# Kernel tuning notes

Measured on AMD Instinct MI355X. Metric: run time of the kernel, lower is better.

## Reference

```python
import jax, jax.numpy as jnp
import numpy as np

NB, T, NS, NC = 512, 128, 32, 16
NSC = NS + NC


def setup_inputs() -> dict:
    key = jax.random.key(0)
    k1, k2, k3, k4, k5, k6 = jax.random.split(key, 6)
    # Q must be PSD per-step (as in the pypose example: Q = Q.mT @ Q), plus a
    # small ridge so Quu is well-conditioned for pinv.
    Qr = jax.random.normal(k1, (NB, T, NSC, NSC), jnp.float32)
    Q = jnp.einsum('btji,btjk->btik', Qr, Qr) / NSC + 0.1 * jnp.eye(NSC, dtype=jnp.float32)
    p = jax.random.normal(k2, (NB, T, NSC), jnp.float32)
    # Mildly stable LTI dynamics so the T=128 rollout stays bounded.
    A0 = 0.5 * jnp.eye(NS, dtype=jnp.float32) + 0.1 * jax.random.normal(k3, (NS, NS), jnp.float32) / np.sqrt(NS)
    A = jnp.broadcast_to(A0, (NB, NS, NS)).astype(jnp.float32)
    Bm = jax.random.normal(k4, (NB, NS, NC), jnp.float32) / np.sqrt(NS)
    c1 = jax.random.normal(k5, (NB, NS), jnp.float32)
    x_init = jax.random.normal(k6, (NB, NS), jnp.float32)
    return {"x_init": x_init, "Q": Q, "p": p, "A": A, "Bm": Bm, "c1": c1}


def _bmv(M, v):
    return jnp.einsum('bij,bj->bi', M, v)


def reference(x_init, Q, p, A, Bm, c1):
    # F = [A B] : [NB, NS, NSC] (time-invariant LTI system)
    F = jnp.concatenate([A, Bm], axis=-1)
    FT = jnp.swapaxes(F, -1, -2)

    Qtm = jnp.moveaxis(Q, 1, 0)  # [T, NB, NSC, NSC]
    ptm = jnp.moveaxis(p, 1, 0)  # [T, NB, NSC]

    # ---- backward Riccati recursion (t = T-1 .. 0) ----
    def bwd_step(carry, inp):
        V, v = carry  # V: [NB,NS,NS], v: [NB,NS]; zero at t = T-1
        Qt_in, pt = inp
        Qt = Qt_in + FT @ V @ F
        qt = pt + _bmv(FT, v) + _bmv(FT, _bmv(V, c1))
        Qxx, Qxu = Qt[..., :NS, :NS], Qt[..., :NS, NS:]
        Qux, Quu = Qt[..., NS:, :NS], Qt[..., NS:, NS:]
        qx, qu = qt[..., :NS], qt[..., NS:]
        Quu_inv = jnp.linalg.pinv(Quu)
        Kt = -(Quu_inv @ Qux)                 # [NB, NC, NS]
        kt = -_bmv(Quu_inv, qu)               # [NB, NC]
        KtT = jnp.swapaxes(Kt, -1, -2)
        V_new = Qxx + Qxu @ Kt + KtT @ Qux + KtT @ Quu @ Kt
        v_new = qx + _bmv(Qxu, kt) + _bmv(KtT, qu) + _bmv(KtT @ Quu, kt)
        return (V_new, v_new), (Kt, kt)

    V0 = jnp.zeros((NB, NS, NS), Q.dtype)
    v0 = jnp.zeros((NB, NS), Q.dtype)
    _, (Ks, ks) = jax.lax.scan(bwd_step, (V0, v0), (Qtm, ptm), reverse=True)

    # ---- forward rollout (t = 0 .. T-1) ----
    def fwd_step(x, inp):
        Kt, kt, Qt, pt = inp
        ut = _bmv(Kt, x) + kt
        xu = jnp.concatenate([x, ut], axis=-1)
        x_next = _bmv(A, x) + _bmv(Bm, ut) + c1
        c = 0.5 * jnp.einsum('bi,bij,bj->b', xu, Qt, xu) + jnp.sum(xu * pt, axis=-1)
        return x_next, (x, ut, c)

    _, (xs, us, cs) = jax.lax.scan(fwd_step, x_init, (Ks, ks, Qtm, ptm))
    x = jnp.moveaxis(xs, 0, 1)   # [NB, T, NS], states x_0..x_{T-1}
    u = jnp.moveaxis(us, 0, 1)   # [NB, T, NC]
    cost = jnp.sum(cs, axis=0)   # [NB]
    return x, u, cost
```

## Files before the change

kernel.cpp:

```cpp
#include <hip/hip_runtime.h>

#define NB 512
#define T 128
#define NS 32
#define NC 16
#define NSC 48
#define PF 52
#define PV 36
#define PK 36

__device__ __forceinline__ float4 ld4(const float* p) { return *(const float4*)p; }
__device__ __forceinline__ void st4(float* p, float4 v) { *(float4*)p = v; }
__device__ __forceinline__ void fma4(float4& a, float s, float4 f) {
    a.x = fmaf(s, f.x, a.x); a.y = fmaf(s, f.y, a.y);
    a.z = fmaf(s, f.z, a.z); a.w = fmaf(s, f.w, a.w);
}
__device__ __forceinline__ float dot4(float4 a, float4 b) {
    return fmaf(a.x, b.x, fmaf(a.y, b.y, fmaf(a.z, b.z, a.w * b.w)));
}

__global__ __launch_bounds__(256, 2)
void lqr_backward(const float* __restrict__ Q,
                  const float* __restrict__ p,
                  const float* __restrict__ A,
                  const float* __restrict__ Bm,
                  const float* __restrict__ c1,
                  float* __restrict__ Kws,
                  float* __restrict__ kws)
{
    const int b = blockIdx.x;
    const int tid = threadIdx.x;
    const int lane = tid & 63;
    const int wv = tid >> 6;

    __shared__ __align__(16) float sF[NS][PF];
    __shared__ __align__(16) float sW[NS][PF];
    __shared__ __align__(16) float sQt[NSC][PF];
    __shared__ __align__(16) float sV[NS][PV];
    __shared__ __align__(16) float sKt[NC][PK];
    __shared__ __align__(16) float sz[NS];
    __shared__ __align__(16) float sqt[NSC];
    __shared__ __align__(16) float sv[NS];
    __shared__ __align__(16) float sc1[NS];
    __shared__ __align__(16) float skt[NC];

    for (int e = tid; e < NS * NSC; e += 256) {
        int i = e / NSC, j = e % NSC;
        sF[i][j] = (j < NS) ? A[(size_t)b * NS * NS + i * NS + j]
                            : Bm[(size_t)b * NS * NC + i * NC + (j - NS)];
    }
    for (int e = tid; e < NS * NS; e += 256) sV[e >> 5][e & 31] = 0.f;
    if (tid < NS) { sv[tid] = 0.f; sc1[tid] = c1[(size_t)b * NS + tid]; }
    __syncthreads();

    for (int t = T - 1; t >= 0; --t) {
        const float* Qg = Q + ((size_t)b * T + t) * NSC * NSC;

        float4 qgb0 = {0,0,0,0}, qgb1 = {0,0,0,0};
        float preg = 0.f;
        if (tid < 96) {
            int i0b = NS + (tid / 12) * 2, j0b = (tid % 12) * 4;
            qgb0 = ld4(Qg + i0b * NSC + j0b);
            qgb1 = ld4(Qg + (i0b + 1) * NSC + j0b);
        }
        if (tid >= 96 && tid < 144) preg = p[((size_t)b * T + t) * NSC + (tid - 96)];
        if (tid < 192) {
            const int i0 = (tid / 12) * 2, j0 = (tid % 12) * 4;
            float4 a0 = {0,0,0,0}, a1 = {0,0,0,0};
            #pragma unroll 8
            for (int k = 0; k < NS; ++k) {
                float2 v2 = *(const float2*)&sV[k][i0];
                float4 f4 = ld4(&sF[k][j0]);
                fma4(a0, v2.x, f4); fma4(a1, v2.y, f4);
            }
            st4(&sW[i0][j0], a0); st4(&sW[i0 + 1][j0], a1);
        } else if (tid < 224) {
            int i = tid - 192;
            float a = sv[i];
            #pragma unroll
            for (int k0 = 0; k0 < NS; k0 += 4)
                a += dot4(ld4(&sV[i][k0]), ld4(&sc1[k0]));
            sz[i] = a;
        }
        __syncthreads();

        float4 qgc0 = {0,0,0,0}, qgc1 = {0,0,0,0};
        int i0c = 0, j0c = 0;
        if (tid >= 64 && tid < 192) {
            int ct = tid - 64; i0c = (ct / 8) * 2; j0c = (ct % 8) * 4;
            qgc0 = ld4(Qg + i0c * NSC + j0c);
            qgc1 = ld4(Qg + (i0c + 1) * NSC + j0c);
        }
        if (tid < 96) {
            const int i0b = NS + (tid / 12) * 2, j0b = (tid % 12) * 4;
            float4 a0 = qgb0, a1 = qgb1;
            #pragma unroll 8
            for (int k = 0; k < NS; ++k) {
                float2 f2 = *(const float2*)&sF[k][i0b];
                float4 w4 = ld4(&sW[k][j0b]);
                fma4(a0, f2.x, w4); fma4(a1, f2.y, w4);
            }
            st4(&sQt[i0b][j0b], a0); st4(&sQt[i0b + 1][j0b], a1);
        } else if (tid < 144) {
            int j = tid - 96;
            float a = preg;
            #pragma unroll 8
            for (int k = 0; k < NS; ++k) a = fmaf(sF[k][j], sz[k], a);
            sqt[j] = a;
        }
        __syncthreads();

        if (wv == 0) {
            float R[NC];
            if (lane < NC) {
                #pragma unroll
                for (int i = 0; i < NC; ++i) R[i] = sQt[NS + i][NS + lane];
            } else if (lane < NSC) {
                #pragma unroll
                for (int i = 0; i < NC; ++i) R[i] = sQt[NS + i][lane - NC];
            } else if (lane == NSC) {
                #pragma unroll
                for (int i = 0; i < NC; ++i) R[i] = sqt[NS + i];
            } else {
                #pragma unroll
                for (int i = 0; i < NC; ++i) R[i] = 0.f;
            }
            #pragma unroll
            for (int k = 0; k < NC; ++k) {
                float pk = __shfl(R[k], k, 64);
                float inv = 1.0f / pk;
                float tm = R[k] * inv;
                #pragma unroll
                for (int i = 0; i < NC; ++i) {
                    if (i == k) continue;
                    float cki = __shfl(R[i], k, 64);
                    R[i] = fmaf(-tm, cki, R[i]);
                }
                R[k] = tm;
            }
            if (lane >= NC && lane < NSC) {
                const int c = lane - NC;
                #pragma unroll
                for (int i = 0; i < NC; ++i) sKt[i][c] = -R[i];
            } else if (lane == NSC) {
                #pragma unroll
                for (int i = 0; i < NC; ++i) skt[i] = -R[i];
            }
        } else if (tid < 192) {
            float4 a0 = qgc0, a1 = qgc1;
            #pragma unroll 8
            for (int k = 0; k < NS; ++k) {
                float2 f2 = *(const float2*)&sF[k][i0c];
                float4 w4 = ld4(&sW[k][j0c]);
                fma4(a0, f2.x, w4); fma4(a1, f2.y, w4);
            }
            st4(&sQt[i0c][j0c], a0); st4(&sQt[i0c + 1][j0c], a1);
        }
        __syncthreads();

        if (tid < 128) {
            const int i0 = (tid / 8) * 2, j0 = (tid % 8) * 4;
            float4 a0 = ld4(&sQt[i0][j0]), a1 = ld4(&sQt[i0 + 1][j0]);
            #pragma unroll
            for (int k = 0; k < NC; ++k) {
                float2 q2 = *(const float2*)&sQt[NS + k][i0];
                float4 k4 = ld4(&sKt[k][j0]);
                fma4(a0, q2.x, k4); fma4(a1, q2.y, k4);
            }
            st4(&sV[i0][j0], a0); st4(&sV[i0 + 1][j0], a1);
        } else if (tid < 160) {
            int j = tid - 128;
            float a = sqt[j];
            #pragma unroll
            for (int k = 0; k < NC; ++k) a = fmaf(sQt[NS + k][j], skt[k], a);
            sv[j] = a;
        } else if (tid < 176) {
            kws[((size_t)b * T + t) * NC + (tid - 160)] = skt[tid - 160];
        } else if (tid >= 192) {
            float4* Kg4 = (float4*)(Kws + ((size_t)b * T + t) * NC * NS);
            int e = (tid - 192) * 2;
            Kg4[e]     = ld4(&sKt[e >> 3][(e & 7) * 4]);
            Kg4[e + 1] = ld4(&sKt[(e + 1) >> 3][((e + 1) & 7) * 4]);
        }
        __syncthreads();
    }
}

__global__ __launch_bounds__(256, 2)
void lqr_forward(const float* __restrict__ x_init,
                 const float* __restrict__ Q,
                 const float* __restrict__ p,
                 const float* __restrict__ A,
                 const float* __restrict__ Bm,
                 const float* __restrict__ c1,
                 const float* __restrict__ Kws,
                 const float* __restrict__ kws,
                 float* __restrict__ out_x,
                 float* __restrict__ out_u,
                 float* __restrict__ out_cost)
{
    const int b = blockIdx.x;
    const int tid = threadIdx.x;
    const int lane = tid & 63;
    const int wv = tid >> 6;

    __shared__ __align__(16) float sK[2][8 * 576];
    __shared__ __align__(16) float sk[2][128];
    __shared__ __align__(16) float sxu[2][8][48];
    __shared__ float sred[4];

    float costAcc = 0.f;
    float4 Freg[12];
    float c1reg = 0.f, xu = 0.f;

    if (wv == 0) {
        const int i = lane & 31;
        const float* Ar = A + (size_t)b * NS * NS + i * NS;
        const float* Br = Bm + (size_t)b * NS * NC + i * NC;
        #pragma unroll
        for (int g = 0; g < 8; ++g) Freg[g] = ld4(Ar + g * 4);
        #pragma unroll
        for (int g = 0; g < 4; ++g) Freg[8 + g] = ld4(Br + g * 4);
        c1reg = c1[(size_t)b * NS + i];
        xu = x_init[(size_t)b * NS + i];
    } else {
        const float4* src = (const float4*)(Kws + (size_t)b * T * NC * NS);
        int ct = tid - 64;
        for (int idx = ct; idx < 1024; idx += 192) {
            int s = idx >> 7, rem = idx & 127, row = rem >> 3, jg = rem & 7;
            st4(&sK[0][s * 576 + row * 36 + jg * 4], src[idx]);
        }
        if (ct < 32) st4(&sk[0][ct * 4], ((const float4*)(kws + (size_t)b * T * NC))[ct]);
    }
    __syncthreads();

    for (int it = 0; it <= 16; ++it) {
        if (wv == 0) {
            if (it < 16) {
                const int buf = it & 1;
                for (int s = 0; s < 8; ++s) {
                    const float* kb = &sK[buf][s * 576 + (lane & 15) * 36];
                    float4 Kq[8];
                    #pragma unroll
                    for (int g = 0; g < 8; ++g) Kq[g] = ld4(kb + g * 4);
                    float ktv = sk[buf][s * 16 + (lane & 15)];

                    float u0 = 0.f, u1 = 0.f;
                    #pragma unroll
                    for (int g = 0; g < 8; ++g) {
                        float x0 = __shfl(xu, 4 * g + 0, 64);
                        float x1 = __shfl(xu, 4 * g + 1, 64);
                        float x2 = __shfl(xu, 4 * g + 2, 64);
                        float x3 = __shfl(xu, 4 * g + 3, 64);
                        u0 = fmaf(Kq[g].x, x0, u0); u1 = fmaf(Kq[g].y, x1, u1);
                        u0 = fmaf(Kq[g].z, x2, u0); u1 = fmaf(Kq[g].w, x3, u1);
                    }
                    if (lane >= NS && lane < NSC) xu = u0 + u1 + ktv;
                    if (lane < NSC) sxu[buf][s][lane] = xu;

                    float a0 = 0.f, a1 = 0.f;
                    #pragma unroll
                    for (int g = 0; g < 12; ++g) {
                        float x0 = __shfl(xu, 4 * g + 0, 64);
                        float x1 = __shfl(xu, 4 * g + 1, 64);
                        float x2 = __shfl(xu, 4 * g + 2, 64);
                        float x3 = __shfl(xu, 4 * g + 3, 64);
                        a0 = fmaf(Freg[g].x, x0, a0); a1 = fmaf(Freg[g].y, x1, a1);
                        a0 = fmaf(Freg[g].z, x2, a0); a1 = fmaf(Freg[g].w, x3, a1);
                    }
                    if (lane < NS) xu = a0 + a1 + c1reg;
                }
            }
        } else {
            const int ct = tid - 64;
            if (it < 15) {
                const int nbuf = (it + 1) & 1;
                const float4* src = (const float4*)(Kws + ((size_t)b * T + (it + 1) * 8) * NC * NS);
                for (int idx = ct; idx < 1024; idx += 192) {
                    int s = idx >> 7, rem = idx & 127, row = rem >> 3, jg = rem & 7;
                    st4(&sK[nbuf][s * 576 + row * 36 + jg * 4], src[idx]);
                }
                if (ct < 32) st4(&sk[nbuf][ct * 4],
                                 ((const float4*)(kws + ((size_t)b * T + (it + 1) * 8) * NC))[ct]);
            }
            if (it >= 1) {
                const int buf = (it - 1) & 1;
                const int c = it - 1;
                for (int s = 0; s < 8; ++s) {
                    const int t = c * 8 + s;
                    const float* Qg = Q + ((size_t)b * T + t) * NSC * NSC;
                    #pragma unroll
                    for (int rr0 = 0; rr0 < 3; ++rr0) {
                        int rr = ct * 3 + rr0;
                        float4 q = ld4(Qg + rr * 4);
                        int i = rr / 12, j0 = (rr % 12) * 4;
                        float4 xv = ld4(&sxu[buf][s][j0]);
                        costAcc = fmaf(0.5f * sxu[buf][s][i], dot4(q, xv), costAcc);
                    }
                    if (ct < NSC) {
                        float xuv = sxu[buf][s][ct];
                        costAcc = fmaf(p[((size_t)b * T + t) * NSC + ct], xuv, costAcc);
                        if (ct < NS) out_x[((size_t)b * T + t) * NS + ct] = xuv;
                        else         out_u[((size_t)b * T + t) * NC + (ct - NS)] = xuv;
                    }
                }
            }
        }
        __syncthreads();
    }

    for (int off = 32; off > 0; off >>= 1)
        costAcc += __shfl_down(costAcc, off, 64);
    if ((tid & 63) == 0) sred[wv] = costAcc;
    __syncthreads();
    if (tid == 0) out_cost[b] = (sred[0] + sred[1]) + (sred[2] + sred[3]);
}

extern "C" void kernel_launch(void* const* d_in, const int* in_sizes, int n_in,
                              void* d_out, int out_size, void* d_ws, size_t ws_size,
                              hipStream_t stream) {
    const float* x_init = (const float*)d_in[0];
    const float* Q      = (const float*)d_in[1];
    const float* p      = (const float*)d_in[2];
    const float* A      = (const float*)d_in[3];
    const float* Bm     = (const float*)d_in[4];
    const float* c1     = (const float*)d_in[5];

    float* out      = (float*)d_out;
    float* out_x    = out;
    float* out_u    = out + (size_t)NB * T * NS;
    float* out_cost = out + (size_t)NB * T * (NS + NC);

    float* Kws = (float*)d_ws;
    float* kws = Kws + (size_t)NB * T * NC * NS;

    lqr_backward<<<NB, 256, 0, stream>>>(Q, p, A, Bm, c1, Kws, kws);
    lqr_forward<<<NB, 256, 0, stream>>>(x_init, Q, p, A, Bm, c1, Kws, kws,
                                        out_x, out_u, out_cost);
}
```

Before: 1.710 ms.

## Compute LQR cost analytically from Riccati values and precompose K·F in forward rollout

The total cost is now derived in the backward pass from the value function (a scalar kappa accumulated each step plus a quadratic form in x_init with V0, v0), so the forward kernel no longer re-reads all of Q and p. The forward recursion precomputes M = K·[A B] and m = K·c1 + k for chunks of four steps on helper waves, letting the serial wave do a single 48-wide matvec per step. The backward matmul thread tiles are widened to 4x4 register blocks with fewer active threads. This removes a full pass over Q in the forward kernel, at the cost of different floating-point rounding for the cost and extra per-step work in the backward kernel.

```diff
diff --git a/kernel.cpp b/kernel.cpp
--- a/kernel.cpp
+++ b/kernel.cpp
@@ -25,8 +25,10 @@
                   const float* __restrict__ A,
                   const float* __restrict__ Bm,
                   const float* __restrict__ c1,
+                  const float* __restrict__ x_init,
                   float* __restrict__ Kws,
-                  float* __restrict__ kws)
+                  float* __restrict__ kws,
+                  float* __restrict__ out_cost)
 {
     const int b = blockIdx.x;
     const int tid = threadIdx.x;
@@ -51,6 +53,7 @@
     }
     for (int e = tid; e < NS * NS; e += 256) sV[e >> 5][e & 31] = 0.f;
     if (tid < NS) { sv[tid] = 0.f; sc1[tid] = c1[(size_t)b * NS + tid]; }
+    float kappa = 0.f, kap1 = 0.f;
     __syncthreads();
 
     for (int t = T - 1; t >= 0; --t) {
@@ -59,37 +62,41 @@
         float4 qgb0 = {0,0,0,0}, qgb1 = {0,0,0,0};
         float preg = 0.f;
         if (tid < 96) {
-            int i0b = NS + (tid / 12) * 2, j0b = (tid % 12) * 4;
-            qgb0 = ld4(Qg + i0b * NSC + j0b);
-            qgb1 = ld4(Qg + (i0b + 1) * NSC + j0b);
-        }
-        if (tid >= 96 && tid < 144) preg = p[((size_t)b * T + t) * NSC + (tid - 96)];
-        if (tid < 192) {
-            const int i0 = (tid / 12) * 2, j0 = (tid % 12) * 4;
-            float4 a0 = {0,0,0,0}, a1 = {0,0,0,0};
+            const int i0 = (tid / 12) * 4, j0 = (tid % 12) * 4;
+            const int i0b = NS + (tid / 12) * 2;
+            qgb0 = ld4(Qg + i0b * NSC + j0);
+            qgb1 = ld4(Qg + (i0b + 1) * NSC + j0);
+            float4 a0 = {0,0,0,0}, a1 = a0, a2 = a0, a3 = a0;
             #pragma unroll 8
             for (int k = 0; k < NS; ++k) {
-                float2 v2 = *(const float2*)&sV[k][i0];
+                float4 v4 = ld4(&sV[k][i0]);
                 float4 f4 = ld4(&sF[k][j0]);
-                fma4(a0, v2.x, f4); fma4(a1, v2.y, f4);
+                fma4(a0, v4.x, f4); fma4(a1, v4.y, f4);
+                fma4(a2, v4.z, f4); fma4(a3, v4.w, f4);
             }
             st4(&sW[i0][j0], a0); st4(&sW[i0 + 1][j0], a1);
-        } else if (tid < 224) {
-            int i = tid - 192;
+            st4(&sW[i0 + 2][j0], a2); st4(&sW[i0 + 3][j0], a3);
+        } else if (tid < 144) {
+            preg = p[((size_t)b * T + t) * NSC + (tid - 96)];
+        } else if (tid >= 192 && tid < 224) {
+            const int i = tid - 192;
             float a = sv[i];
             #pragma unroll
-            for (int k0 = 0; k0 < NS; k0 += 4)
-                a += dot4(ld4(&sV[i][k0]), ld4(&sc1[k0]));
+            for (int j4 = 0; j4 < NS; j4 += 4)
+                a += dot4(ld4(&sV[i][j4]), ld4(&sc1[j4]));
             sz[i] = a;
         }
         __syncthreads();
 
-        float4 qgc0 = {0,0,0,0}, qgc1 = {0,0,0,0};
+        float4 qx0 = {0,0,0,0}, qx1 = qx0, qx2 = qx0, qx3 = qx0;
         int i0c = 0, j0c = 0;
-        if (tid >= 64 && tid < 192) {
-            int ct = tid - 64; i0c = (ct / 8) * 2; j0c = (ct % 8) * 4;
-            qgc0 = ld4(Qg + i0c * NSC + j0c);
-            qgc1 = ld4(Qg + (i0c + 1) * NSC + j0c);
+        if (tid >= 64 && tid < 128) {
+            const int ct = tid - 64;
+            i0c = (ct >> 3) * 4; j0c = (ct & 7) * 4;
+            qx0 = ld4(Qg + (i0c + 0) * NSC + j0c);
+            qx1 = ld4(Qg + (i0c + 1) * NSC + j0c);
+            qx2 = ld4(Qg + (i0c + 2) * NSC + j0c);
+            qx3 = ld4(Qg + (i0c + 3) * NSC + j0c);
         }
         if (tid < 96) {
             const int i0b = NS + (tid / 12) * 2, j0b = (tid % 12) * 4;
@@ -102,7 +109,7 @@
             }
             st4(&sQt[i0b][j0b], a0); st4(&sQt[i0b + 1][j0b], a1);
         } else if (tid < 144) {
-            int j = tid - 96;
+            const int j = tid - 96;
             float a = preg;
             #pragma unroll 8
             for (int k = 0; k < NS; ++k) a = fmaf(sF[k][j], sz[k], a);
@@ -139,181 +146,244 @@
                 R[k] = tm;
             }
             if (lane >= NC && lane < NSC) {
-                const int c = lane - NC;
-                #pragma unroll
-                for (int i = 0; i < NC; ++i) sKt[i][c] = -R[i];
+                const int cc = lane - NC;
+                #pragma unroll
+                for (int i = 0; i < NC; ++i) sKt[i][cc] = -R[i];
             } else if (lane == NSC) {
                 #pragma unroll
                 for (int i = 0; i < NC; ++i) skt[i] = -R[i];
             }
-        } else if (tid < 192) {
-            float4 a0 = qgc0, a1 = qgc1;
+        } else if (tid < 128) {
+            float4 a0 = qx0, a1 = qx1, a2 = qx2, a3 = qx3;
             #pragma unroll 8
             for (int k = 0; k < NS; ++k) {
-                float2 f2 = *(const float2*)&sF[k][i0c];
+                float4 f4 = ld4(&sF[k][i0c]);
                 float4 w4 = ld4(&sW[k][j0c]);
-                fma4(a0, f2.x, w4); fma4(a1, f2.y, w4);
+                fma4(a0, f4.x, w4); fma4(a1, f4.y, w4);
+                fma4(a2, f4.z, w4); fma4(a3, f4.w, w4);
             }
             st4(&sQt[i0c][j0c], a0); st4(&sQt[i0c + 1][j0c], a1);
+            st4(&sQt[i0c + 2][j0c], a2); st4(&sQt[i0c + 3][j0c], a3);
+        } else if (tid == 224) {
+            float a = 0.f;
+            for (int i = 0; i < NS; ++i) a = fmaf(sc1[i], sv[i] + sz[i], a);
+            kap1 = 0.5f * a;
         }
         __syncthreads();
 
-        if (tid < 128) {
-            const int i0 = (tid / 8) * 2, j0 = (tid % 8) * 4;
-            float4 a0 = ld4(&sQt[i0][j0]), a1 = ld4(&sQt[i0 + 1][j0]);
+        if (tid < 64) {
+            const int i0 = (tid >> 3) * 4, j0 = (tid & 7) * 4;
+            float4 a0 = ld4(&sQt[i0][j0]),     a1 = ld4(&sQt[i0 + 1][j0]);
+            float4 a2 = ld4(&sQt[i0 + 2][j0]), a3 = ld4(&sQt[i0 + 3][j0]);
             #pragma unroll
             for (int k = 0; k < NC; ++k) {
-                float2 q2 = *(const float2*)&sQt[NS + k][i0];
+                float4 q4 = ld4(&sQt[NS + k][i0]);
                 float4 k4 = ld4(&sKt[k][j0]);
-                fma4(a0, q2.x, k4); fma4(a1, q2.y, k4);
+                fma4(a0, q4.x, k4); fma4(a1, q4.y, k4);
+                fma4(a2, q4.z, k4); fma4(a3, q4.w, k4);
             }
             st4(&sV[i0][j0], a0); st4(&sV[i0 + 1][j0], a1);
-        } else if (tid < 160) {
-            int j = tid - 128;
+            st4(&sV[i0 + 2][j0], a2); st4(&sV[i0 + 3][j0], a3);
+        } else if (tid < 96) {
+            const int j = tid - 64;
             float a = sqt[j];
             #pragma unroll
             for (int k = 0; k < NC; ++k) a = fmaf(sQt[NS + k][j], skt[k], a);
             sv[j] = a;
+        } else if (tid < 160) {
+            float4* Kg4 = (float4*)(Kws + ((size_t)b * T + t) * NC * NS);
+            const int e = (tid - 96) * 2;
+            Kg4[e]     = ld4(&sKt[e >> 3][(e & 7) * 4]);
+            Kg4[e + 1] = ld4(&sKt[(e + 1) >> 3][((e + 1) & 7) * 4]);
         } else if (tid < 176) {
             kws[((size_t)b * T + t) * NC + (tid - 160)] = skt[tid - 160];
-        } else if (tid >= 192) {
-            float4* Kg4 = (float4*)(Kws + ((size_t)b * T + t) * NC * NS);
-            int e = (tid - 192) * 2;
-            Kg4[e]     = ld4(&sKt[e >> 3][(e & 7) * 4]);
-            Kg4[e + 1] = ld4(&sKt[(e + 1) >> 3][((e + 1) & 7) * 4]);
+        } else if (tid == 224) {
+            float s2 = 0.f;
+            for (int i = 0; i < NC; ++i) s2 = fmaf(sqt[NS + i], skt[i], s2);
+            kappa += kap1 + 0.5f * s2;
         }
         __syncthreads();
+    }
+
+    if (tid < NS) sz[tid] = x_init[(size_t)b * NS + tid];
+    __syncthreads();
+    if (tid < NS) {
+        float y = 0.f;
+        #pragma unroll
+        for (int j4 = 0; j4 < NS; j4 += 4)
+            y += dot4(ld4(&sV[tid][j4]), ld4(&sz[j4]));
+        sqt[tid] = sz[tid] * (0.5f * y + sv[tid]);
+    }
+    __syncthreads();
+    if (tid == 224) {
+        float cst = kappa;
+        for (int i = 0; i < NS; ++i) cst += sqt[i];
+        out_cost[b] = cst;
     }
 }
 
 __global__ __launch_bounds__(256, 2)
 void lqr_forward(const float* __restrict__ x_init,
-                 const float* __restrict__ Q,
-                 const float* __restrict__ p,
                  const float* __restrict__ A,
                  const float* __restrict__ Bm,
                  const float* __restrict__ c1,
                  const float* __restrict__ Kws,
                  const float* __restrict__ kws,
                  float* __restrict__ out_x,
-                 float* __restrict__ out_u,
-                 float* __restrict__ out_cost)
+                 float* __restrict__ out_u)
 {
     const int b = blockIdx.x;
     const int tid = threadIdx.x;
     const int lane = tid & 63;
     const int wv = tid >> 6;
 
-    __shared__ __align__(16) float sK[2][8 * 576];
-    __shared__ __align__(16) float sk[2][128];
-    __shared__ __align__(16) float sxu[2][8][48];
-    __shared__ float sred[4];
-
-    float costAcc = 0.f;
-    float4 Freg[12];
-    float c1reg = 0.f, xu = 0.f;
-
+    __shared__ __align__(16) float sKT[2][4][32][20];
+    __shared__ __align__(16) float sM[2][4][16][52];
+    __shared__ float sm[2][4][16];
+    __shared__ float skv[2][4][16];
+    __shared__ __align__(16) float sFf[NS][PF];
+    __shared__ float sc1f[NS];
+
+    for (int e = tid; e < NS * NSC; e += 256) {
+        int i = e / NSC, j = e % NSC;
+        sFf[i][j] = (j < NS) ? A[(size_t)b * NS * NS + i * NS + j]
+                             : Bm[(size_t)b * NS * NC + i * NC + (j - NS)];
+    }
+    if (tid < NS) sc1f[tid] = c1[(size_t)b * NS + tid];
+
+    float c[48];
+    float z = 0.f, cr = 0.f;
     if (wv == 0) {
-        const int i = lane & 31;
-        const float* Ar = A + (size_t)b * NS * NS + i * NS;
-        const float* Br = Bm + (size_t)b * NS * NC + i * NC;
-        #pragma unroll
-        for (int g = 0; g < 8; ++g) Freg[g] = ld4(Ar + g * 4);
-        #pragma unroll
-        for (int g = 0; g < 4; ++g) Freg[8 + g] = ld4(Br + g * 4);
-        c1reg = c1[(size_t)b * NS + i];
-        xu = x_init[(size_t)b * NS + i];
-    } else {
-        const float4* src = (const float4*)(Kws + (size_t)b * T * NC * NS);
-        int ct = tid - 64;
-        for (int idx = ct; idx < 1024; idx += 192) {
-            int s = idx >> 7, rem = idx & 127, row = rem >> 3, jg = rem & 7;
-            st4(&sK[0][s * 576 + row * 36 + jg * 4], src[idx]);
-        }
-        if (ct < 32) st4(&sk[0][ct * 4], ((const float4*)(kws + (size_t)b * T * NC))[ct]);
+        if (lane < NS) {
+            const float* Ar = A + (size_t)b * NS * NS + lane * NS;
+            const float* Br = Bm + (size_t)b * NS * NC + lane * NC;
+            #pragma unroll
+            for (int g = 0; g < 8; ++g) {
+                float4 v = ld4(Ar + 4 * g);
+                c[4*g] = v.x; c[4*g+1] = v.y; c[4*g+2] = v.z; c[4*g+3] = v.w;
+            }
+            #pragma unroll
+            for (int g = 0; g < 4; ++g) {
+                float4 v = ld4(Br + 4 * g);
+                c[32+4*g] = v.x; c[33+4*g] = v.y; c[34+4*g] = v.z; c[35+4*g] = v.w;
+            }
+            cr = c1[(size_t)b * NS + lane];
+            z = x_init[(size_t)b * NS + lane];
+        } else if (lane < NSC) {
+            const float* Kr = Kws + (size_t)b * T * NC * NS + (lane - NS) * NS;
+            #pragma unroll
+            for (int g = 0; g < 8; ++g) {
+                float4 v = ld4(Kr + 4 * g);
+                c[4*g] = v.x; c[4*g+1] = v.y; c[4*g+2] = v.z; c[4*g+3] = v.w;
+            }
+            #pragma unroll
+            for (int j = 32; j < 48; ++j) c[j] = 0.f;
+            cr = kws[(size_t)b * T * NC + (lane - NS)];
+        } else {
+            #pragma unroll
+            for (int j = 0; j < 48; ++j) c[j] = 0.f;
+        }
     }
     __syncthreads();
 
-    for (int it = 0; it <= 16; ++it) {
+    for (int i = 0; i < 34; ++i) {
         if (wv == 0) {
-            if (it < 16) {
-                const int buf = it & 1;
-                for (int s = 0; s < 8; ++s) {
-                    const float* kb = &sK[buf][s * 576 + (lane & 15) * 36];
-                    float4 Kq[8];
+            if (i == 0) {
+                float acc[4] = {0,0,0,0};
+                #pragma unroll
+                for (int j = 0; j < NS; ++j) {
+                    float zb = __shfl(z, j, 64);
+                    acc[j & 3] = fmaf(c[j], zb, acc[j & 3]);
+                }
+                float u0 = (acc[0] + acc[1]) + (acc[2] + acc[3]) + cr;
+                if (lane >= NS && lane < NSC) z = u0;
+                if (lane < NS) out_x[((size_t)b * T) * NS + lane] = z;
+                else if (lane < NSC) out_u[((size_t)b * T) * NC + (lane - NS)] = z;
+            } else if (i >= 2) {
+                const int cch = i - 2, ring = cch & 1;
+                #pragma unroll
+                for (int sl = 0; sl < 4; ++sl) {
+                    const int s = cch * 4 + sl;
+                    if (s == 0) continue;
+                    if (lane >= NS && lane < NSC) {
+                        const float* mr = &sM[ring][sl][lane - NS][0];
+                        #pragma unroll
+                        for (int g = 0; g < 12; ++g) {
+                            float4 v = ld4(mr + 4 * g);
+                            c[4*g] = v.x; c[4*g+1] = v.y; c[4*g+2] = v.z; c[4*g+3] = v.w;
+                        }
+                        cr = sm[ring][sl][lane - NS];
+                    }
+                    float acc[4] = {0,0,0,0};
                     #pragma unroll
-                    for (int g = 0; g < 8; ++g) Kq[g] = ld4(kb + g * 4);
-                    float ktv = sk[buf][s * 16 + (lane & 15)];
-
-                    float u0 = 0.f, u1 = 0.f;
-                    #pragma unroll
-                    for (int g = 0; g < 8; ++g) {
-                        float x0 = __shfl(xu, 4 * g + 0, 64);
-                        float x1 = __shfl(xu, 4 * g + 1, 64);
-                        float x2 = __shfl(xu, 4 * g + 2, 64);
-                        float x3 = __shfl(xu, 4 * g + 3, 64);
-                        u0 = fmaf(Kq[g].x, x0, u0); u1 = fmaf(Kq[g].y, x1, u1);
-                        u0 = fmaf(Kq[g].z, x2, u0); u1 = fmaf(Kq[g].w, x3, u1);
+                    for (int j = 0; j < NSC; ++j) {
+                        float zb = __shfl(z, j, 64);
+                        acc[j & 3] = fmaf(c[j], zb, acc[j & 3]);
                     }
-                    if (lane >= NS && lane < NSC) xu = u0 + u1 + ktv;
-                    if (lane < NSC) sxu[buf][s][lane] = xu;
-
-                    float a0 = 0.f, a1 = 0.f;
-                    #pragma unroll
-                    for (int g = 0; g < 12; ++g) {
-                        float x0 = __shfl(xu, 4 * g + 0, 64);
-                        float x1 = __shfl(xu, 4 * g + 1, 64);
-                        float x2 = __shfl(xu, 4 * g + 2, 64);
-                        float x3 = __shfl(xu, 4 * g + 3, 64);
-                        a0 = fmaf(Freg[g].x, x0, a0); a1 = fmaf(Freg[g].y, x1, a1);
-                        a0 = fmaf(Freg[g].z, x2, a0); a1 = fmaf(Freg[g].w, x3, a1);
-                    }
-                    if (lane < NS) xu = a0 + a1 + c1reg;
+                    float zn = (acc[0] + acc[1]) + (acc[2] + acc[3]) + cr;
+                    if (lane < NSC) z = zn;
+                    if (lane < NS) out_x[((size_t)b * T + s) * NS + lane] = z;
+                    else if (lane < NSC) out_u[((size_t)b * T + s) * NC + (lane - NS)] = z;
                 }
             }
         } else {
             const int ct = tid - 64;
-            if (it < 15) {
-                const int nbuf = (it + 1) & 1;
-                const float4* src = (const float4*)(Kws + ((size_t)b * T + (it + 1) * 8) * NC * NS);
-                for (int idx = ct; idx < 1024; idx += 192) {
-                    int s = idx >> 7, rem = idx & 127, row = rem >> 3, jg = rem & 7;
-                    st4(&sK[nbuf][s * 576 + row * 36 + jg * 4], src[idx]);
-                }
-                if (ct < 32) st4(&sk[nbuf][ct * 4],
-                                 ((const float4*)(kws + ((size_t)b * T + (it + 1) * 8) * NC))[ct]);
-            }
-            if (it >= 1) {
-                const int buf = (it - 1) & 1;
-                const int c = it - 1;
-                for (int s = 0; s < 8; ++s) {
-                    const int t = c * 8 + s;
-                    const float* Qg = Q + ((size_t)b * T + t) * NSC * NSC;
-                    #pragma unroll
-                    for (int rr0 = 0; rr0 < 3; ++rr0) {
-                        int rr = ct * 3 + rr0;
-                        float4 q = ld4(Qg + rr * 4);
-                        int i = rr / 12, j0 = (rr % 12) * 4;
-                        float4 xv = ld4(&sxu[buf][s][j0]);
-                        costAcc = fmaf(0.5f * sxu[buf][s][i], dot4(q, xv), costAcc);
+            if (i < 32) {
+                const int ring = i & 1;
+                const float* Kg = Kws + ((size_t)b * T + i * 4) * NC * NS;
+                #pragma unroll
+                for (int rep = 0; rep < 3; ++rep) {
+                    const int idx = ct + rep * 192;
+                    if (idx < 512) {
+                        float4 kv = ld4(Kg + idx * 4);
+                        const int sl = idx >> 7, rem = idx & 127;
+                        const int r = rem >> 3, c4 = (rem & 7) * 4;
+                        sKT[ring][sl][c4 + 0][r] = kv.x;
+                        sKT[ring][sl][c4 + 1][r] = kv.y;
+                        sKT[ring][sl][c4 + 2][r] = kv.z;
+                        sKT[ring][sl][c4 + 3][r] = kv.w;
                     }
-                    if (ct < NSC) {
-                        float xuv = sxu[buf][s][ct];
-                        costAcc = fmaf(p[((size_t)b * T + t) * NSC + ct], xuv, costAcc);
-                        if (ct < NS) out_x[((size_t)b * T + t) * NS + ct] = xuv;
-                        else         out_u[((size_t)b * T + t) * NC + (ct - NS)] = xuv;
+                }
+                if (ct < 16) {
+                    float4 kv = ld4(kws + ((size_t)b * T + i * 4 + (ct >> 2)) * NC + (ct & 3) * 4);
+                    const int sl = ct >> 2, c4 = (ct & 3) * 4;
+                    skv[ring][sl][c4 + 0] = kv.x; skv[ring][sl][c4 + 1] = kv.y;
+                    skv[ring][sl][c4 + 2] = kv.z; skv[ring][sl][c4 + 3] = kv.w;
+                }
+            }
+            if (i >= 1 && i <= 32) {
+                const int cch = i - 1, ring = cch & 1;
+                if (ct < 96) {
+                    const int sl = ct / 24, rem = ct % 24;
+                    const int r0 = (rem / 6) * 4, j0 = (rem % 6) * 8;
+                    float4 a00 = {0,0,0,0}, a01 = a00, a10 = a00, a11 = a00;
+                    float4 a20 = a00, a21 = a00, a30 = a00, a31 = a00;
+                    #pragma unroll 8
+                    for (int k = 0; k < NS; ++k) {
+                        float4 kk = ld4(&sKT[ring][sl][k][r0]);
+                        float4 f0 = ld4(&sFf[k][j0]);
+                        float4 f1 = ld4(&sFf[k][j0 + 4]);
+                        fma4(a00, kk.x, f0); fma4(a01, kk.x, f1);
+                        fma4(a10, kk.y, f0); fma4(a11, kk.y, f1);
+                        fma4(a20, kk.z, f0); fma4(a21, kk.z, f1);
+                        fma4(a30, kk.w, f0); fma4(a31, kk.w, f1);
                     }
+                    st4(&sM[ring][sl][r0 + 0][j0], a00); st4(&sM[ring][sl][r0 + 0][j0 + 4], a01);
+                    st4(&sM[ring][sl][r0 + 1][j0], a10); st4(&sM[ring][sl][r0 + 1][j0 + 4], a11);
+                    st4(&sM[ring][sl][r0 + 2][j0], a20); st4(&sM[ring][sl][r0 + 2][j0 + 4], a21);
+                    st4(&sM[ring][sl][r0 + 3][j0], a30); st4(&sM[ring][sl][r0 + 3][j0 + 4], a31);
+                } else if (ct < 160) {
+                    const int id = ct - 96, sl = id >> 4, r = id & 15;
+                    float a = skv[ring][sl][r];
+                    #pragma unroll 8
+                    for (int k = 0; k < NS; ++k)
+                        a = fmaf(sKT[ring][sl][k][r], sc1f[k], a);
+                    sm[ring][sl][r] = a;
                 }
             }
         }
         __syncthreads();
     }
-
-    for (int off = 32; off > 0; off >>= 1)
-        costAcc += __shfl_down(costAcc, off, 64);
-    if ((tid & 63) == 0) sred[wv] = costAcc;
-    __syncthreads();
-    if (tid == 0) out_cost[b] = (sred[0] + sred[1]) + (sred[2] + sred[3]);
 }
 
 extern "C" void kernel_launch(void* const* d_in, const int* in_sizes, int n_in,
@@ -334,7 +404,6 @@
     float* Kws = (float*)d_ws;
     float* kws = Kws + (size_t)NB * T * NC * NS;
 
-    lqr_backward<<<NB, 256, 0, stream>>>(Q, p, A, Bm, c1, Kws, kws);
-    lqr_forward<<<NB, 256, 0, stream>>>(x_init, Q, p, A, Bm, c1, Kws, kws,
-                                        out_x, out_u, out_cost);
+    lqr_backward<<<NB, 256, 0, stream>>>(Q, p, A, Bm, c1, x_init, Kws, kws, out_cost);
+    lqr_forward<<<NB, 256, 0, stream>>>(x_init, A, Bm, c1, Kws, kws, out_x, out_u);
 }
```

Result: slower. 1.807 ms (+5.7%).
